# Performance work log

Hardware: AMD Instinct MI355X
Metric: run time of the kernel (lower is better)

## Reference

```python
import jax, jax.numpy as jnp
import numpy as np


def setup_inputs() -> dict:
    key = jax.random.key(0)
    ks = jax.random.split(key, 7)
    n, L = 8, 1024
    s = 64            # input_size_1 = input_size_2 = 64
    d = s + 1         # 65, after bias-ones concat / h feature size
    inp = {
        "layer1": jax.random.normal(ks[0], (n, L, s), dtype=jnp.float32),
        "layer2": jax.random.normal(ks[1], (n, L, s), dtype=jnp.float32),
        "layer3": jax.random.normal(ks[2], (n, L, s), dtype=jnp.float32),
        "h1": jax.random.normal(ks[3], (n, L, d), dtype=jnp.float32),
        "h2": jax.random.normal(ks[4], (n, L, d), dtype=jnp.float32),
        "h3": jax.random.normal(ks[5], (n, L, d), dtype=jnp.float32),
        # quartic core W (xavier-normal-ish scale): shape (s1+1, s2+1, s2+1, s2+1)
        "W": jax.random.normal(ks[6], (d, d, d, d), dtype=jnp.float32) * 0.02,
    }
    return inp


def reference(layer1, layer2, layer3, h1, h2, h3, W):
    # Non-factorized, flag=True, 3D-input path of Qriaffine.forward:
    #   out = einsum('nia,abcd,njb,nic,njd->nij', [layer1;1], W, [layer2;1], h1, h2)
    # layer3 / h3 are unused in this branch (but layer3 is still concatenated
    # with ones in the original code, a no-op for the output).
    n, L, _ = layer1.shape
    ones = jnp.ones((n, L, 1), dtype=layer1.dtype)
    l1 = jnp.concatenate([layer1, ones], axis=-1)  # [n, L, d]
    l2 = jnp.concatenate([layer2, ones], axis=-1)  # [n, L, d]
    # efficient contraction order, avoiding the huge [n,L,d,d,d] intermediate:
    p = l1[..., :, None] * h1[..., None, :]          # niac: [n, L, d, d]
    q = jnp.einsum('niac,abcd->nibd', p, W)          # [n, L, d, d]
    r = l2[..., :, None] * h2[..., None, :]          # njbd: [n, L, d, d]
    out = jnp.einsum('nibd,njbd->nij', q, r)         # [n, L, L]
    return out
```

## Files before the change

### kernel.cpp

```cpp
#include <hip/hip_runtime.h>
#include <hip/hip_bf16.h>


typedef __attribute__((ext_vector_type(8))) short short8;
typedef __attribute__((ext_vector_type(4))) float floatx4;

#define KP 4256
#define DP 4352
#define NROW 8192

__device__ __forceinline__ void async_ld16(const void* g, void* l) {
  __builtin_amdgcn_global_load_lds(
      (const __attribute__((address_space(1))) unsigned int*)g,
      (__attribute__((address_space(3))) unsigned int*)l, 16, 0, 0);
}

__global__ void zero_kernel(float4* __restrict__ p, long n) {
  long i = (long)blockIdx.x * blockDim.x + threadIdx.x;
  long stride = (long)gridDim.x * blockDim.x;
  float4 z = make_float4(0.f, 0.f, 0.f, 0.f);
  for (; i < n; i += stride) p[i] = z;
}

__global__ void build_wt2(const float* __restrict__ W, __hip_bfloat16* __restrict__ Wt2) {
  __shared__ __hip_bfloat16 tile[65 * 66];
  const int a = blockIdx.x, b = blockIdx.y;
  const float* src = W + (size_t)(a * 65 + b) * 4225;
  for (int idx = threadIdx.x; idx < 4225; idx += 256) {
    int c = idx / 65, d = idx - c * 65;
    tile[d * 66 + c] = __float2bfloat16(src[idx]);
  }
  __syncthreads();
  for (int idx = threadIdx.x; idx < 4225; idx += 256) {
    int d = idx / 65, c = idx - d * 65;
    Wt2[(size_t)(b * 65 + d) * KP + a * 65 + c] = tile[d * 66 + c];
  }
}

__global__ void build_p(const float* __restrict__ layer, const float* __restrict__ h,
                        __hip_bfloat16* __restrict__ P, int width) {
  const int row = blockIdx.x;
  __shared__ float lv[65], hv[65];
  if (threadIdx.x < 64) lv[threadIdx.x] = layer[(size_t)row * 64 + threadIdx.x];
  if (threadIdx.x == 64) lv[64] = 1.0f;
  if (threadIdx.x < 65) hv[threadIdx.x] = h[(size_t)row * 65 + threadIdx.x];
  __syncthreads();
  for (int base = threadIdx.x * 8; base < width; base += 256 * 8) {
    alignas(16) __hip_bfloat16 tmp[8];
#pragma unroll
    for (int j = 0; j < 8; ++j) {
      int idx = base + j;
      float v = 0.f;
      if (idx < 4225) {
        int x = idx / 65, y = idx - x * 65;
        v = lv[x] * hv[y];
      }
      tmp[j] = __float2bfloat16(v);
    }
    *(float4*)(P + (size_t)row * width + base) = *(const float4*)tmp;
  }
}

template <int STORE_BF16>
__global__ __launch_bounds__(256) void gemm_nt(
    const __hip_bfloat16* __restrict__ A, const __hip_bfloat16* __restrict__ B,
    void* __restrict__ Cv, int K, int lda, int ldb, int ldc,
    long sA, long sB, long sC) {
  __shared__ alignas(16) __hip_bfloat16 As[128 * 32];
  __shared__ alignas(16) __hip_bfloat16 Bs[128 * 32];
  const int z = blockIdx.z;
  A += (long)z * sA;
  B += (long)z * sB;
  const int bm = blockIdx.y * 128;
  const int bn = blockIdx.x * 128;
  const int t = threadIdx.x;
  const int lane = t & 63;
  const int wave = t >> 6;
  const int quad = lane >> 4;
  const int lrow = lane & 15;
  const int wm = (wave >> 1) * 64;
  const int wn = (wave & 1) * 64;

  const int L0 = t, L1 = t + 256;
  const int r0 = L0 >> 2, sg0 = (L0 & 3) ^ (r0 & 3);
  const int r1 = L1 >> 2, sg1 = (L1 & 3) ^ (r1 & 3);
  const __hip_bfloat16* ga0 = A + (size_t)(bm + r0) * lda + sg0 * 8;
  const __hip_bfloat16* ga1 = A + (size_t)(bm + r1) * lda + sg1 * 8;
  const __hip_bfloat16* gb0 = B + (size_t)(bn + r0) * ldb + sg0 * 8;
  const __hip_bfloat16* gb1 = B + (size_t)(bn + r1) * ldb + sg1 * 8;
  __hip_bfloat16* lA0 = As + (size_t)(wave * 64) * 8;
  __hip_bfloat16* lA1 = As + (size_t)(256 + wave * 64) * 8;
  __hip_bfloat16* lB0 = Bs + (size_t)(wave * 64) * 8;
  __hip_bfloat16* lB1 = Bs + (size_t)(256 + wave * 64) * 8;

  const int slq = (quad ^ (lrow & 3)) * 8;

  floatx4 acc[4][4] = {};

  for (int k0 = 0; k0 < K; k0 += 32) {
    __syncthreads();
    async_ld16(ga0 + k0, lA0);
    async_ld16(ga1 + k0, lA1);
    async_ld16(gb0 + k0, lB0);
    async_ld16(gb1 + k0, lB1);
    __syncthreads();

    short8 af[4], bf[4];
#pragma unroll
    for (int i = 0; i < 4; ++i) {
      af[i] = *(const short8*)(&As[(wm + i * 16 + lrow) * 32 + slq]);
      bf[i] = *(const short8*)(&Bs[(wn + i * 16 + lrow) * 32 + slq]);
    }
#pragma unroll
    for (int mi = 0; mi < 4; ++mi)
#pragma unroll
      for (int nj = 0; nj < 4; ++nj)
        acc[mi][nj] = __builtin_amdgcn_mfma_f32_16x16x32_bf16(af[mi], bf[nj], acc[mi][nj], 0, 0, 0);
  }

  if (STORE_BF16) {
    __hip_bfloat16* C = (__hip_bfloat16*)Cv + (long)z * sC;
#pragma unroll
    for (int mi = 0; mi < 4; ++mi)
#pragma unroll
      for (int nj = 0; nj < 4; ++nj)
#pragma unroll
        for (int r = 0; r < 4; ++r) {
          int row = bm + wm + mi * 16 + quad * 4 + r;
          int col = bn + wn + nj * 16 + lrow;
          C[(size_t)row * ldc + col] = __float2bfloat16(acc[mi][nj][r]);
        }
  } else {
    float* C = (float*)Cv + (long)z * sC;
#pragma unroll
    for (int mi = 0; mi < 4; ++mi)
#pragma unroll
      for (int nj = 0; nj < 4; ++nj)
#pragma unroll
        for (int r = 0; r < 4; ++r) {
          int row = bm + wm + mi * 16 + quad * 4 + r;
          int col = bn + wn + nj * 16 + lrow;
          C[(size_t)row * ldc + col] = acc[mi][nj][r];
        }
  }
}

extern "C" void kernel_launch(void* const* d_in, const int* in_sizes, int n_in,
                              void* d_out, int out_size, void* d_ws, size_t ws_size,
                              hipStream_t stream) {
  const float* layer1 = (const float*)d_in[0];
  const float* layer2 = (const float*)d_in[1];
  const float* h1 = (const float*)d_in[3];
  const float* h2 = (const float*)d_in[4];
  const float* W = (const float*)d_in[6];
  float* out = (float*)d_out;

  char* ws = (char*)d_ws;
  __hip_bfloat16* P = (__hip_bfloat16*)(ws);
  __hip_bfloat16* Wt2 = (__hip_bfloat16*)(ws + 69730304ULL);
  __hip_bfloat16* Q = (__hip_bfloat16*)(ws + 106774528ULL);
  __hip_bfloat16* R = (__hip_bfloat16*)(ws + 178077696ULL);

  zero_kernel<<<2048, 256, 0, stream>>>((float4*)Wt2, (long)DP * KP * 2 / 16);
  build_wt2<<<dim3(65, 65), 256, 0, stream>>>(W, Wt2);
  build_p<<<NROW, 256, 0, stream>>>(layer1, h1, P, KP);
  build_p<<<NROW, 256, 0, stream>>>(layer2, h2, R, DP);
  gemm_nt<1><<<dim3(DP / 128, NROW / 128, 1), 256, 0, stream>>>(
      P, Wt2, Q, KP, KP, KP, DP, 0, 0, 0);
  gemm_nt<0><<<dim3(1024 / 128, 1024 / 128, 8), 256, 0, stream>>>(
      Q, R, out, DP, DP, DP, 1024, 1024L * DP, 1024L * DP, 1024L * 1024);
}
```

Measured before the change: 692.5 us.

## Switch GEMM to 32x32x16 MFMA with K-tile 64 and reuse workspace for R

The shared GEMM kernel now uses 32x32x16 bf16 MFMA instructions on a 64-wide K tile instead of 16x16x32 on a 32-wide tile. The LDS swizzle is widened to 8 segments, and each stage does four async loads per operand. Fewer barriers per K and larger MFMA tiles are meant to cut synchronisation and LDS read overhead. KP is padded to 4288 (a multiple of 64), and R now reuses P's workspace, so building R is moved after the first GEMM, which makes the two stages strictly sequential.

Result: faster. 612.1 us (-11.6%).

```diff
diff --git a/kernel.cpp b/kernel.cpp
--- a/kernel.cpp
+++ b/kernel.cpp
@@ -3,9 +3,9 @@
 
 
 typedef __attribute__((ext_vector_type(8))) short short8;
-typedef __attribute__((ext_vector_type(4))) float floatx4;
+typedef __attribute__((ext_vector_type(16))) float floatx16;
 
-#define KP 4256
+#define KP 4288
 #define DP 4352
 #define NROW 8192
 
@@ -66,8 +66,8 @@
     const __hip_bfloat16* __restrict__ A, const __hip_bfloat16* __restrict__ B,
     void* __restrict__ Cv, int K, int lda, int ldb, int ldc,
     long sA, long sB, long sC) {
-  __shared__ alignas(16) __hip_bfloat16 As[128 * 32];
-  __shared__ alignas(16) __hip_bfloat16 Bs[128 * 32];
+  __shared__ alignas(16) __hip_bfloat16 As[128 * 64];
+  __shared__ alignas(16) __hip_bfloat16 Bs[128 * 64];
   const int z = blockIdx.z;
   A += (long)z * sA;
   B += (long)z * sB;
@@ -76,71 +76,78 @@
   const int t = threadIdx.x;
   const int lane = t & 63;
   const int wave = t >> 6;
-  const int quad = lane >> 4;
-  const int lrow = lane & 15;
+  const int l31 = lane & 31;
+  const int lhi = lane >> 5;
   const int wm = (wave >> 1) * 64;
   const int wn = (wave & 1) * 64;
 
-  const int L0 = t, L1 = t + 256;
-  const int r0 = L0 >> 2, sg0 = (L0 & 3) ^ (r0 & 3);
-  const int r1 = L1 >> 2, sg1 = (L1 & 3) ^ (r1 & 3);
-  const __hip_bfloat16* ga0 = A + (size_t)(bm + r0) * lda + sg0 * 8;
-  const __hip_bfloat16* ga1 = A + (size_t)(bm + r1) * lda + sg1 * 8;
-  const __hip_bfloat16* gb0 = B + (size_t)(bn + r0) * ldb + sg0 * 8;
-  const __hip_bfloat16* gb1 = B + (size_t)(bn + r1) * ldb + sg1 * 8;
-  __hip_bfloat16* lA0 = As + (size_t)(wave * 64) * 8;
-  __hip_bfloat16* lA1 = As + (size_t)(256 + wave * 64) * 8;
-  __hip_bfloat16* lB0 = Bs + (size_t)(wave * 64) * 8;
-  __hip_bfloat16* lB1 = Bs + (size_t)(256 + wave * 64) * 8;
+  const __hip_bfloat16* gA[4];
+  const __hip_bfloat16* gB[4];
+  __hip_bfloat16* lA[4];
+  __hip_bfloat16* lB[4];
+#pragma unroll
+  for (int r = 0; r < 4; ++r) {
+    int L = r * 256 + t;
+    int row = L >> 3, sl = L & 7;
+    int sg = sl ^ (row & 7);
+    gA[r] = A + (size_t)(bm + row) * lda + sg * 8;
+    gB[r] = B + (size_t)(bn + row) * ldb + sg * 8;
+    lA[r] = As + (size_t)(r * 256 + wave * 64) * 8;
+    lB[r] = Bs + (size_t)(r * 256 + wave * 64) * 8;
+  }
 
-  const int slq = (quad ^ (lrow & 3)) * 8;
+  const int x7 = l31 & 7;
+  const int rA0 = (wm + l31) * 64, rA1 = (wm + 32 + l31) * 64;
+  const int rB0 = (wn + l31) * 64, rB1 = (wn + 32 + l31) * 64;
 
-  floatx4 acc[4][4] = {};
+  floatx16 acc[2][2] = {};
 
-  for (int k0 = 0; k0 < K; k0 += 32) {
+  for (int k0 = 0; k0 < K; k0 += 64) {
     __syncthreads();
-    async_ld16(ga0 + k0, lA0);
-    async_ld16(ga1 + k0, lA1);
-    async_ld16(gb0 + k0, lB0);
-    async_ld16(gb1 + k0, lB1);
+#pragma unroll
+    for (int r = 0; r < 4; ++r) {
+      async_ld16(gA[r] + k0, lA[r]);
+      async_ld16(gB[r] + k0, lB[r]);
+    }
     __syncthreads();
 
-    short8 af[4], bf[4];
 #pragma unroll
-    for (int i = 0; i < 4; ++i) {
-      af[i] = *(const short8*)(&As[(wm + i * 16 + lrow) * 32 + slq]);
-      bf[i] = *(const short8*)(&Bs[(wn + i * 16 + lrow) * 32 + slq]);
+    for (int ks = 0; ks < 4; ++ks) {
+      const int pc = ((ks * 2 + lhi) ^ x7) * 8;
+      short8 a0 = *(const short8*)(&As[rA0 + pc]);
+      short8 a1 = *(const short8*)(&As[rA1 + pc]);
+      short8 b0 = *(const short8*)(&Bs[rB0 + pc]);
+      short8 b1 = *(const short8*)(&Bs[rB1 + pc]);
+      acc[0][0] = __builtin_amdgcn_mfma_f32_32x32x16_bf16(a0, b0, acc[0][0], 0, 0, 0);
+      acc[0][1] = __builtin_amdgcn_mfma_f32_32x32x16_bf16(a0, b1, acc[0][1], 0, 0, 0);
+      acc[1][0] = __builtin_amdgcn_mfma_f32_32x32x16_bf16(a1, b0, acc[1][0], 0, 0, 0);
+      acc[1][1] = __builtin_amdgcn_mfma_f32_32x32x16_bf16(a1, b1, acc[1][1], 0, 0, 0);
     }
-#pragma unroll
-    for (int mi = 0; mi < 4; ++mi)
-#pragma unroll
-      for (int nj = 0; nj < 4; ++nj)
-        acc[mi][nj] = __builtin_amdgcn_mfma_f32_16x16x32_bf16(af[mi], bf[nj], acc[mi][nj], 0, 0, 0);
   }
 
   if (STORE_BF16) {
     __hip_bfloat16* C = (__hip_bfloat16*)Cv + (long)z * sC;
 #pragma unroll
-    for (int mi = 0; mi < 4; ++mi)
+    for (int mt = 0; mt < 2; ++mt)
 #pragma unroll
-      for (int nj = 0; nj < 4; ++nj)
+      for (int nt = 0; nt < 2; ++nt)
 #pragma unroll
-        for (int r = 0; r < 4; ++r) {
-          int row = bm + wm + mi * 16 + quad * 4 + r;
-          int col = bn + wn + nj * 16 + lrow;
-          C[(size_t)row * ldc + col] = __float2bfloat16(acc[mi][nj][r]);
+        for (int reg = 0; reg < 16; ++reg) {
+          int row = bm + wm + mt * 32 + (reg & 3) + 8 * (reg >> 2) + 4 * lhi;
+          int col = bn + wn + nt * 32 + l31;
+          C[(size_t)row * ldc + col] = __float2bfloat16(acc[mt][nt][reg]);
         }
   } else {
     float* C = (float*)Cv + (long)z * sC;
 #pragma unroll
-    for (int mi = 0; mi < 4; ++mi)
+    for (int mt = 0; mt < 2; ++mt)
 #pragma unroll
-      for (int nj = 0; nj < 4; ++nj)
+      for (int nt = 0; nt < 2; ++nt)
 #pragma unroll
-        for (int r = 0; r < 4; ++r) {
-          int row = bm + wm + mi * 16 + quad * 4 + r;
-          int col = bn + wn + nj * 16 + lrow;
-          C[(size_t)row * ldc + col] = acc[mi][nj][r];
+        for (int reg = 0; reg < 16; ++reg) {
+          int row = bm + wm + mt * 32 + (reg & 3) + 8 * (reg >> 2) + 4 * lhi;
+          int col = bn + wn + nt * 32 + l31;
+          C[(size_t)row * ldc + col] = acc[mt][nt][reg];
         }
   }
 }
@@ -157,16 +164,16 @@
 
   char* ws = (char*)d_ws;
   __hip_bfloat16* P = (__hip_bfloat16*)(ws);
-  __hip_bfloat16* Wt2 = (__hip_bfloat16*)(ws + 69730304ULL);
-  __hip_bfloat16* Q = (__hip_bfloat16*)(ws + 106774528ULL);
-  __hip_bfloat16* R = (__hip_bfloat16*)(ws + 178077696ULL);
+  __hip_bfloat16* Wt2 = (__hip_bfloat16*)(ws + 70254592ULL);
+  __hip_bfloat16* Q = (__hip_bfloat16*)(ws + 107577344ULL);
+  __hip_bfloat16* R = (__hip_bfloat16*)(ws);
 
   zero_kernel<<<2048, 256, 0, stream>>>((float4*)Wt2, (long)DP * KP * 2 / 16);
   build_wt2<<<dim3(65, 65), 256, 0, stream>>>(W, Wt2);
   build_p<<<NROW, 256, 0, stream>>>(layer1, h1, P, KP);
-  build_p<<<NROW, 256, 0, stream>>>(layer2, h2, R, DP);
   gemm_nt<1><<<dim3(DP / 128, NROW / 128, 1), 256, 0, stream>>>(
       P, Wt2, Q, KP, KP, KP, DP, 0, 0, 0);
+  build_p<<<NROW, 256, 0, stream>>>(layer2, h2, R, DP);
   gemm_nt<0><<<dim3(1024 / 128, 1024 / 128, 8), 256, 0, stream>>>(
       Q, R, out, DP, DP, DP, 1024, 1024L * DP, 1024L * DP, 1024L * 1024);
 }
```
